# Performance work log

Measured on AMD Instinct MI355X. Metric: run time of the kernel, lower is better.

Reference implementation:

```python
import jax, jax.numpy as jnp
import numpy as np

VP = 0.4
EP = 0.21

def _c_matrix():
    # Faithfully replicate the original Ci (including its asymmetric rows 2) and invert.
    Ci = np.zeros((6, 6), dtype=np.float64)
    Ci[0, 0] = 1 / EP; Ci[0, 1] = -VP / EP; Ci[0, 2] = -VP / EP
    Ci[1, 0] = -VP / EP; Ci[1, 1] = 1 / EP; Ci[1, 2] = -VP / EP
    Ci[2, 0] = -VP;      Ci[2, 1] = -VP;      Ci[2, 2] = 1 / EP
    Ci[3, 3] = 2 * (1 + VP) / EP
    Ci[4, 4] = 2 * (1 + VP) / EP
    Ci[5, 5] = 2 * (1 + VP) / EP
    return np.linalg.inv(Ci).astype(np.float32)

C_MAT = jnp.asarray(_c_matrix())
N = 12288

def setup_inputs() -> dict:
    key = jax.random.key(0)
    k1, k2, k3 = jax.random.split(key, 3)
    xyz = jax.random.normal(k1, (N, 3), dtype=jnp.float32)
    new_xyz = jax.random.normal(k2, (N, 3), dtype=jnp.float32)
    # ~half the points are 'inside' (gt_sdf < 1e-8)
    gt_sdf = jax.random.uniform(k3, (N,), dtype=jnp.float32) - 0.5
    return {"new_xyz": new_xyz, "xyz": xyz, "gt_sdf": gt_sdf}

def reference(new_xyz, xyz, gt_sdf):
    motion = new_xyz - xyz                      # [N,3]
    inside = gt_sdf < 1e-8                      # [N] bool, selects inside points
    w = new_xyz                                 # warped coordinates (KNN space)
    n = w.shape[0]
    # Brute-force NN among inside points (KDTree k=2, second neighbor == nearest non-self).
    sq = jnp.sum(w * w, axis=1)                 # [N]
    d2 = sq[:, None] + sq[None, :] - 2.0 * (w @ w.T)   # [N,N] squared distances
    BIG = jnp.float32(1e30)
    bad_col = (~inside)[None, :] | jnp.eye(n, dtype=bool)
    d2 = jnp.where(bad_col, BIG, d2)
    nn_idx = jnp.argmin(d2, axis=1)             # nearest inside neighbor (excluding self)
    nn_d = jnp.sqrt(jnp.maximum(jnp.min(d2, axis=1), 0.0))
    # tree_list1 filter: drop rows whose nearest neighbor is a duplicate point
    valid = inside & (nn_d > 1e-8)              # [N]
    dm = motion[nn_idx] - motion                # motion_delta
    dc = w[nn_idx] - w + 1e-8                   # cords_delta (+1e-8 as in original)
    v = valid[:, None]
    dm = jnp.where(v, dm, 0.0)                  # neutralize masked rows (keep shapes static)
    dc = jnp.where(v, dc, 1.0)
    du, dv, dw = dm[:, 0], dm[:, 1], dm[:, 2]
    dx, dy, dz = dc[:, 0], dc[:, 1], dc[:, 2]
    et = jnp.stack([du / dx, dv / dy, dw / dz,
                    (du / dy + dv / dx) / 2,
                    (du / dz + dw / dx) / 2,
                    (dw / dy + dv / dz) / 2], axis=1)   # [N,6] strain tensor
    # diag(et @ C @ et.T) as an O(N) batched quadratic form
    q = jnp.einsum('ni,ij,nj->n', et, C_MAT, et)
    q = jnp.where(valid, q, 0.0)
    n_valid = jnp.sum(valid).astype(jnp.float32)
    return jnp.linalg.norm(q) / n_valid
```

## Files before the change

### kernel.cpp

```cpp
#include <hip/hip_runtime.h>
#include <math.h>
#include <string.h>

#define N 12288
#define QP 7168
#define TILE 128
#define NSPLIT 56
#define ACCS 2
#define QBLK 512
#define NQB 14
#define BT 1024
#define BB 12
#define NPART (QP / 256)

typedef unsigned long long ull;

struct CMat { float c[6][6]; };

__global__ __launch_bounds__(1024) void build_kernel(
    const float* __restrict__ new_xyz,
    const float* __restrict__ gt_sdf,
    float4* __restrict__ pts,
    int* __restrict__ cj,
    int* __restrict__ Mout,
    ull* __restrict__ best,
    unsigned int* __restrict__ ticket)
{
    const int tid = threadIdx.x;
    const int b = blockIdx.x;
    const int lane = tid & 63;
    const int wave = tid >> 6;

    int cpre = 0;
    #pragma unroll
    for (int r = 0; r < BB - 1; ++r) {
        const float sv = (r < b) ? gt_sdf[r * BT + tid] : 1.0f;
        cpre += (sv < 1e-8f) ? 1 : 0;
    }
    #pragma unroll
    for (int off = 32; off > 0; off >>= 1)
        cpre += __shfl_down(cpre, off, 64);

    const int idx = b * BT + tid;
    const float px = new_xyz[3 * idx + 0];
    const float py = new_xyz[3 * idx + 1];
    const float pz = new_xyz[3 * idx + 2];
    const bool ins = gt_sdf[idx] < 1e-8f;
    const ull m = __ballot(ins);
    const int rank = __popcll(m & ((1ull << lane) - 1ull));

    __shared__ int wpre[16];
    __shared__ int wcnt[16];
    __shared__ int woff[16];
    __shared__ int tot_s;
    if (lane == 0) { wpre[wave] = cpre; wcnt[wave] = __popcll(m); }
    __syncthreads();
    if (tid == 0) {
        int cb = 0;
        for (int w = 0; w < 16; ++w) cb += wpre[w];
        int run = cb;
        for (int w = 0; w < 16; ++w) { woff[w] = run; run += wcnt[w]; }
        tot_s = run;
    }
    __syncthreads();

    const int slot = woff[wave] + rank;
    if (ins && slot < QP) {
        pts[slot] = make_float4(-2.0f * px, -2.0f * py, -2.0f * pz,
                                px * px + py * py + pz * pz);
        cj[slot] = idx;
    }

    const int gid = b * BT + tid;
    if (gid < QP) best[gid] = ~0ull;
    if (gid == 0) *ticket = 0u;

    if (b == BB - 1) {
        const int M = tot_s;
        if (tid == 0) *Mout = M;
        for (int s = M + tid; s < QP; s += BT)
            pts[s] = make_float4(0.0f, 0.0f, 0.0f, 3e30f);
    }
}

template<bool CAREFUL>
__device__ __forceinline__ void nn_inner(
    const float4* __restrict__ tile,
    const float* wx, const float* wy, const float* wz,
    const int* kx,
    float* bd, int* bk)
{
    #pragma unroll 8
    for (int k = 0; k < TILE; ++k) {
        const float4 b = tile[k];
        #pragma unroll
        for (int a = 0; a < ACCS; ++a) {
            float t = fmaf(wz[a], b.z, b.w);
            t = fmaf(wy[a], b.y, t);
            t = fmaf(wx[a], b.x, t);
            bool ok = t < bd[a];
            if (CAREFUL) ok = ok && (k != kx[a]);
            if (ok) { bd[a] = t; bk[a] = k; }
        }
    }
}

__global__ __launch_bounds__(256, 4) void nn_kernel(
    const float4* __restrict__ pts,
    const int* __restrict__ Mptr,
    ull* __restrict__ best)
{
    const int tid = threadIdx.x;
    const int qbase = blockIdx.x * QBLK;
    const int s = blockIdx.y;
    const int jb = s * TILE;

    const int M = *Mptr;
    if (jb >= M || qbase >= M) return;

    float wx[ACCS], wy[ACCS], wz[ACCS];
    int kx[ACCS];
    #pragma unroll
    for (int a = 0; a < ACCS; ++a) {
        const int ci = qbase + tid + a * 256;
        const float4 q = pts[ci];
        wx[a] = -0.5f * q.x;
        wy[a] = -0.5f * q.y;
        wz[a] = -0.5f * q.z;
        kx[a] = ci - jb;
    }

    __shared__ float4 tile[TILE];
    if (tid < TILE) tile[tid] = pts[jb + tid];
    __syncthreads();

    float bd[ACCS];
    int bk[ACCS];
    #pragma unroll
    for (int a = 0; a < ACCS; ++a) { bd[a] = 3.0e38f; bk[a] = 0; }

    const bool dirty = (jb < qbase + QBLK) && (jb + TILE > qbase);
    if (dirty)
        nn_inner<true>(tile, wx, wy, wz, kx, bd, bk);
    else
        nn_inner<false>(tile, wx, wy, wz, kx, bd, bk);

    #pragma unroll
    for (int a = 0; a < ACCS; ++a) {
        const int ci = qbase + tid + a * 256;
        unsigned u = __float_as_uint(bd[a]);
        u = ((int)u < 0) ? ~u : (u | 0x80000000u);
        const ull v = ((ull)u << 32) | (ull)(unsigned)(jb + bk[a]);
        atomicMin(&best[ci], v);
    }
}

__global__ __launch_bounds__(256) void loss_kernel(
    const float* __restrict__ new_xyz,
    const float* __restrict__ xyz,
    const int* __restrict__ cj,
    const int* __restrict__ Mptr,
    const ull* __restrict__ best_arr,
    double* __restrict__ partial_sum,
    unsigned int* __restrict__ partial_cnt,
    unsigned int* __restrict__ ticket,
    float* __restrict__ out,
    CMat C)
{
    const int tid = threadIdx.x;
    const int ci = blockIdx.x * 256 + tid;

    const ull best = best_arr[ci];
    const int M = *Mptr;
    const bool real = (ci < M);

    const unsigned u = (unsigned)(best >> 32);
    const unsigned bits = (u & 0x80000000u) ? (u ^ 0x80000000u) : ~u;
    const float key = __uint_as_float(bits);
    const int cc = real ? (int)(unsigned)(best & 0xffffffffu) : 0;

    const int i  = real ? cj[ci] : 0;
    const int nn = cj[cc];

    const float wix = new_xyz[3 * i + 0];
    const float wiy = new_xyz[3 * i + 1];
    const float wiz = new_xyz[3 * i + 2];
    const float sqi = wix * wix + wiy * wiy + wiz * wiz;

    const float d2 = sqi + key;
    const float nnd = sqrtf(fmaxf(d2, 0.0f));
    const bool valid = real && (nnd > 1e-8f);

    float q = 0.0f;
    if (valid) {
        const float xix = xyz[3 * i + 0], xiy = xyz[3 * i + 1], xiz = xyz[3 * i + 2];
        const float wnx = new_xyz[3 * nn + 0], wny = new_xyz[3 * nn + 1], wnz = new_xyz[3 * nn + 2];
        const float xnx = xyz[3 * nn + 0],     xny = xyz[3 * nn + 1],     xnz = xyz[3 * nn + 2];

        const float du = (wnx - xnx) - (wix - xix);
        const float dv = (wny - xny) - (wiy - xiy);
        const float dw = (wnz - xnz) - (wiz - xiz);
        const float dx = wnx - wix + 1e-8f;
        const float dy = wny - wiy + 1e-8f;
        const float dz = wnz - wiz + 1e-8f;

        float et[6];
        et[0] = du / dx;
        et[1] = dv / dy;
        et[2] = dw / dz;
        et[3] = (du / dy + dv / dx) * 0.5f;
        et[4] = (du / dz + dw / dx) * 0.5f;
        et[5] = (dw / dy + dv / dz) * 0.5f;

        #pragma unroll
        for (int a = 0; a < 6; ++a) {
            float s2 = 0.0f;
            #pragma unroll
            for (int b2 = 0; b2 < 6; ++b2) s2 += C.c[a][b2] * et[b2];
            q += et[a] * s2;
        }
    }

    double q2 = (double)q * (double)q;
    #pragma unroll
    for (int off = 32; off > 0; off >>= 1)
        q2 += __shfl_down(q2, off, 64);
    const ull vm = __ballot(valid);
    const int lane = tid & 63;
    const int wid = tid >> 6;

    __shared__ double wsum[4];
    __shared__ unsigned wcnt2[4];
    __shared__ bool sdone;
    if (lane == 0) { wsum[wid] = q2; wcnt2[wid] = (unsigned)__popcll(vm); }
    __syncthreads();
    if (tid == 0) {
        partial_sum[blockIdx.x] = wsum[0] + wsum[1] + wsum[2] + wsum[3];
        partial_cnt[blockIdx.x] = wcnt2[0] + wcnt2[1] + wcnt2[2] + wcnt2[3];
        __threadfence();
        const unsigned t = atomicAdd(ticket, 1u);
        sdone = (t == NPART - 1);
    }
    __syncthreads();

    if (sdone && tid < 64) {
        __threadfence();
        double s = (tid < NPART) ? partial_sum[tid] : 0.0;
        double c = (tid < NPART) ? (double)partial_cnt[tid] : 0.0;
        #pragma unroll
        for (int off = 32; off > 0; off >>= 1) {
            s += __shfl_down(s, off, 64);
            c += __shfl_down(c, off, 64);
        }
        if (tid == 0) out[0] = (float)(sqrt(s) / c);
    }
}

static void build_cmat(CMat* M)
{
    const double VP = 0.4, EP = 0.21;
    double A[6][12];
    memset(A, 0, sizeof(A));
    double Ci[6][6];
    memset(Ci, 0, sizeof(Ci));
    Ci[0][0] = 1.0 / EP; Ci[0][1] = -VP / EP; Ci[0][2] = -VP / EP;
    Ci[1][0] = -VP / EP; Ci[1][1] = 1.0 / EP; Ci[1][2] = -VP / EP;
    Ci[2][0] = -VP;      Ci[2][1] = -VP;      Ci[2][2] = 1.0 / EP;
    Ci[3][3] = 2.0 * (1.0 + VP) / EP;
    Ci[4][4] = Ci[3][3];
    Ci[5][5] = Ci[3][3];

    for (int i = 0; i < 6; ++i) {
        for (int j = 0; j < 6; ++j) A[i][j] = Ci[i][j];
        A[i][6 + i] = 1.0;
    }
    for (int col = 0; col < 6; ++col) {
        int piv = col;
        for (int r = col + 1; r < 6; ++r)
            if (fabs(A[r][col]) > fabs(A[piv][col])) piv = r;
        if (piv != col)
            for (int c = 0; c < 12; ++c) { double t = A[col][c]; A[col][c] = A[piv][c]; A[piv][c] = t; }
        const double d = A[col][col];
        for (int c = 0; c < 12; ++c) A[col][c] /= d;
        for (int r = 0; r < 6; ++r) {
            if (r == col) continue;
            const double f = A[r][col];
            if (f == 0.0) continue;
            for (int c = 0; c < 12; ++c) A[r][c] -= f * A[col][c];
        }
    }
    for (int i = 0; i < 6; ++i)
        for (int j = 0; j < 6; ++j)
            M->c[i][j] = (float)A[i][6 + j];
}

extern "C" void kernel_launch(void* const* d_in, const int* in_sizes, int n_in,
                              void* d_out, int out_size, void* d_ws, size_t ws_size,
                              hipStream_t stream)
{
    const float* new_xyz = (const float*)d_in[0];
    const float* xyz     = (const float*)d_in[1];
    const float* gt_sdf  = (const float*)d_in[2];
    float* out = (float*)d_out;

    char* p = (char*)d_ws;
    float4* pts = (float4*)p;                    p += (size_t)QP * 16;
    int* cj = (int*)p;                           p += (size_t)QP * 4;
    int* Mptr = (int*)p;                         p += 16;
    ull* best = (ull*)p;                         p += (size_t)QP * 8;
    double* partial_sum = (double*)p;            p += NPART * sizeof(double);
    unsigned int* partial_cnt = (unsigned int*)p; p += NPART * sizeof(unsigned int);
    unsigned int* ticket = (unsigned int*)p;

    CMat C;
    build_cmat(&C);

    build_kernel<<<BB, BT, 0, stream>>>(new_xyz, gt_sdf, pts, cj, Mptr, best, ticket);
    nn_kernel<<<dim3(NQB, NSPLIT), 256, 0, stream>>>(pts, Mptr, best);
    loss_kernel<<<QP / 256, 256, 0, stream>>>(new_xyz, xyz, cj, Mptr, best,
                                              partial_sum, partial_cnt, ticket,
                                              out, C);
}
```

Baseline: 76.95 us.

## Fuse nearest-neighbour and loss kernels with a global-counter grid barrier

Merges the brute-force NN search kernel and the loss/reduction kernel into one launch. Every block increments a global ticket after its atomicMin updates, and the first NPART blocks spin-wait until all blocks have arrived before computing the loss. This removes one kernel launch and its inter-kernel gap. It relies on all blocks being co-resident and adds spin-wait traffic, with a guard that could break out early.

New measurement: 93.86 us. +22.0%, slower.

```diff
diff --git a/kernel.cpp b/kernel.cpp
--- a/kernel.cpp
+++ b/kernel.cpp
@@ -9,6 +9,7 @@
 #define ACCS 2
 #define QBLK 512
 #define NQB 14
+#define NBLK (NQB * NSPLIT)
 #define BT 1024
 #define BB 12
 #define NPART (QP / 256)
@@ -24,7 +25,8 @@
     int* __restrict__ cj,
     int* __restrict__ Mout,
     ull* __restrict__ best,
-    unsigned int* __restrict__ ticket)
+    unsigned int* __restrict__ ticket2,
+    unsigned int* __restrict__ ticket3)
 {
     const int tid = threadIdx.x;
     const int b = blockIdx.x;
@@ -73,7 +75,7 @@
 
     const int gid = b * BT + tid;
     if (gid < QP) best[gid] = ~0ull;
-    if (gid == 0) *ticket = 0u;
+    if (gid == 0) { *ticket2 = 0u; *ticket3 = 0u; }
 
     if (b == BB - 1) {
         const int M = tot_s;
@@ -105,79 +107,92 @@
     }
 }
 
-__global__ __launch_bounds__(256, 4) void nn_kernel(
-    const float4* __restrict__ pts,
-    const int* __restrict__ Mptr,
-    ull* __restrict__ best)
-{
-    const int tid = threadIdx.x;
-    const int qbase = blockIdx.x * QBLK;
-    const int s = blockIdx.y;
-    const int jb = s * TILE;
-
-    const int M = *Mptr;
-    if (jb >= M || qbase >= M) return;
-
-    float wx[ACCS], wy[ACCS], wz[ACCS];
-    int kx[ACCS];
-    #pragma unroll
-    for (int a = 0; a < ACCS; ++a) {
-        const int ci = qbase + tid + a * 256;
-        const float4 q = pts[ci];
-        wx[a] = -0.5f * q.x;
-        wy[a] = -0.5f * q.y;
-        wz[a] = -0.5f * q.z;
-        kx[a] = ci - jb;
-    }
-
-    __shared__ float4 tile[TILE];
-    if (tid < TILE) tile[tid] = pts[jb + tid];
-    __syncthreads();
-
-    float bd[ACCS];
-    int bk[ACCS];
-    #pragma unroll
-    for (int a = 0; a < ACCS; ++a) { bd[a] = 3.0e38f; bk[a] = 0; }
-
-    const bool dirty = (jb < qbase + QBLK) && (jb + TILE > qbase);
-    if (dirty)
-        nn_inner<true>(tile, wx, wy, wz, kx, bd, bk);
-    else
-        nn_inner<false>(tile, wx, wy, wz, kx, bd, bk);
-
-    #pragma unroll
-    for (int a = 0; a < ACCS; ++a) {
-        const int ci = qbase + tid + a * 256;
-        unsigned u = __float_as_uint(bd[a]);
-        u = ((int)u < 0) ? ~u : (u | 0x80000000u);
-        const ull v = ((ull)u << 32) | (ull)(unsigned)(jb + bk[a]);
-        atomicMin(&best[ci], v);
-    }
-}
-
-__global__ __launch_bounds__(256) void loss_kernel(
+__global__ __launch_bounds__(256, 4) void nn_loss_kernel(
     const float* __restrict__ new_xyz,
     const float* __restrict__ xyz,
+    const float4* __restrict__ pts,
     const int* __restrict__ cj,
     const int* __restrict__ Mptr,
-    const ull* __restrict__ best_arr,
+    ull* __restrict__ best,
+    unsigned int* __restrict__ ticket2,
+    unsigned int* __restrict__ ticket3,
     double* __restrict__ partial_sum,
     unsigned int* __restrict__ partial_cnt,
-    unsigned int* __restrict__ ticket,
     float* __restrict__ out,
     CMat C)
 {
     const int tid = threadIdx.x;
-    const int ci = blockIdx.x * 256 + tid;
-
-    const ull best = best_arr[ci];
+    const int f = blockIdx.x;
+    const int qb = f % NQB;
+    const int s = f / NQB;
+    const int qbase = qb * QBLK;
+    const int jb = s * TILE;
     const int M = *Mptr;
+
+    if (jb < M && qbase < M) {
+        float wx[ACCS], wy[ACCS], wz[ACCS];
+        int kx[ACCS];
+        #pragma unroll
+        for (int a = 0; a < ACCS; ++a) {
+            const int ci = qbase + tid + a * 256;
+            const float4 q = pts[ci];
+            wx[a] = -0.5f * q.x;
+            wy[a] = -0.5f * q.y;
+            wz[a] = -0.5f * q.z;
+            kx[a] = ci - jb;
+        }
+
+        __shared__ float4 tile[TILE];
+        if (tid < TILE) tile[tid] = pts[jb + tid];
+        __syncthreads();
+
+        float bd[ACCS];
+        int bk[ACCS];
+        #pragma unroll
+        for (int a = 0; a < ACCS; ++a) { bd[a] = 3.0e38f; bk[a] = 0; }
+
+        const bool dirty = (jb < qbase + QBLK) && (jb + TILE > qbase);
+        if (dirty)
+            nn_inner<true>(tile, wx, wy, wz, kx, bd, bk);
+        else
+            nn_inner<false>(tile, wx, wy, wz, kx, bd, bk);
+
+        #pragma unroll
+        for (int a = 0; a < ACCS; ++a) {
+            const int ci = qbase + tid + a * 256;
+            unsigned u = __float_as_uint(bd[a]);
+            u = ((int)u < 0) ? ~u : (u | 0x80000000u);
+            const ull v = ((ull)u << 32) | (ull)(unsigned)(jb + bk[a]);
+            atomicMin(&best[ci], v);
+        }
+    }
+
+    __syncthreads();
+    if (tid == 0) {
+        __threadfence();
+        __hip_atomic_fetch_add(ticket2, 1u, __ATOMIC_RELEASE,
+                               __HIP_MEMORY_SCOPE_AGENT);
+    }
+    if (f >= NPART) return;
+
+    if (tid == 0) {
+        long long guard = 0;
+        while (__hip_atomic_load(ticket2, __ATOMIC_ACQUIRE,
+                                 __HIP_MEMORY_SCOPE_AGENT) < (unsigned)NBLK) {
+            __builtin_amdgcn_s_sleep(8);
+            if (++guard > (1ll << 28)) break;
+        }
+    }
+    __syncthreads();
+
+    const int ci = f * 256 + tid;
+    const ull b64 = best[ci];
     const bool real = (ci < M);
 
-    const unsigned u = (unsigned)(best >> 32);
+    const unsigned u = (unsigned)(b64 >> 32);
     const unsigned bits = (u & 0x80000000u) ? (u ^ 0x80000000u) : ~u;
     const float key = __uint_as_float(bits);
-    const int cc = real ? (int)(unsigned)(best & 0xffffffffu) : 0;
+    const int cc = real ? (int)(unsigned)(b64 & 0xffffffffu) : 0;
 
     const int i  = real ? cj[ci] : 0;
     const int nn = cj[cc];
@@ -235,24 +250,24 @@
     if (lane == 0) { wsum[wid] = q2; wcnt2[wid] = (unsigned)__popcll(vm); }
     __syncthreads();
     if (tid == 0) {
-        partial_sum[blockIdx.x] = wsum[0] + wsum[1] + wsum[2] + wsum[3];
-        partial_cnt[blockIdx.x] = wcnt2[0] + wcnt2[1] + wcnt2[2] + wcnt2[3];
+        partial_sum[f] = wsum[0] + wsum[1] + wsum[2] + wsum[3];
+        partial_cnt[f] = wcnt2[0] + wcnt2[1] + wcnt2[2] + wcnt2[3];
         __threadfence();
-        const unsigned t = atomicAdd(ticket, 1u);
+        const unsigned t = atomicAdd(ticket3, 1u);
         sdone = (t == NPART - 1);
     }
     __syncthreads();
 
     if (sdone && tid < 64) {
         __threadfence();
-        double s = (tid < NPART) ? partial_sum[tid] : 0.0;
-        double c = (tid < NPART) ? (double)partial_cnt[tid] : 0.0;
+        double ss = (tid < NPART) ? partial_sum[tid] : 0.0;
+        double cc2 = (tid < NPART) ? (double)partial_cnt[tid] : 0.0;
         #pragma unroll
         for (int off = 32; off > 0; off >>= 1) {
-            s += __shfl_down(s, off, 64);
-            c += __shfl_down(c, off, 64);
-        }
-        if (tid == 0) out[0] = (float)(sqrt(s) / c);
+            ss += __shfl_down(ss, off, 64);
+            cc2 += __shfl_down(cc2, off, 64);
+        }
+        if (tid == 0) out[0] = (float)(sqrt(ss) / cc2);
     }
 }
 
@@ -310,14 +325,15 @@
     ull* best = (ull*)p;                         p += (size_t)QP * 8;
     double* partial_sum = (double*)p;            p += NPART * sizeof(double);
     unsigned int* partial_cnt = (unsigned int*)p; p += NPART * sizeof(unsigned int);
-    unsigned int* ticket = (unsigned int*)p;
+    unsigned int* ticket2 = (unsigned int*)p;    p += sizeof(unsigned int);
+    unsigned int* ticket3 = (unsigned int*)p;
 
     CMat C;
     build_cmat(&C);
 
-    build_kernel<<<BB, BT, 0, stream>>>(new_xyz, gt_sdf, pts, cj, Mptr, best, ticket);
-    nn_kernel<<<dim3(NQB, NSPLIT), 256, 0, stream>>>(pts, Mptr, best);
-    loss_kernel<<<QP / 256, 256, 0, stream>>>(new_xyz, xyz, cj, Mptr, best,
-                                              partial_sum, partial_cnt, ticket,
-                                              out, C);
-}
+    build_kernel<<<BB, BT, 0, stream>>>(new_xyz, gt_sdf, pts, cj, Mptr, best,
+                                        ticket2, ticket3);
+    nn_loss_kernel<<<NBLK, 256, 0, stream>>>(new_xyz, xyz, pts, cj, Mptr, best,
+                                             ticket2, ticket3,
+                                             partial_sum, partial_cnt, out, C);
+}
```

## Fuse NN search and loss into one kernel with per-block stripe reduction

Applied to the files above, without the earlier changes.

Merges the brute-force nearest-neighbour kernel and the loss kernel into a single launch. Each block now handles 32 queries, and 8 groups of 32 threads each scan a 896-point stripe, reading candidate points straight from global memory instead of a shared tile. Stripe results are reduced in shared memory, which removes the global atomicMin array, its initialisation and one kernel launch. The trade-off is fewer blocks (224) and one query per thread with no register reuse across queries, so the scan may be limited by memory latency or load throughput.

Measured after the change: 149.1 us. 93.7% more time.

```diff
diff --git a/kernel.cpp b/kernel.cpp
--- a/kernel.cpp
+++ b/kernel.cpp
@@ -4,14 +4,12 @@
 
 #define N 12288
 #define QP 7168
-#define TILE 128
-#define NSPLIT 56
-#define ACCS 2
-#define QBLK 512
-#define NQB 14
 #define BT 1024
 #define BB 12
-#define NPART (QP / 256)
+#define G2 224
+#define QG 32
+#define NST 8
+#define SL 896
 
 typedef unsigned long long ull;
 
@@ -23,7 +21,6 @@
     float4* __restrict__ pts,
     int* __restrict__ cj,
     int* __restrict__ Mout,
-    ull* __restrict__ best,
     unsigned int* __restrict__ ticket)
 {
     const int tid = threadIdx.x;
@@ -71,9 +68,7 @@
         cj[slot] = idx;
     }
 
-    const int gid = b * BT + tid;
-    if (gid < QP) best[gid] = ~0ull;
-    if (gid == 0) *ticket = 0u;
+    if (b == 0 && tid == 0) *ticket = 0u;
 
     if (b == BB - 1) {
         const int M = tot_s;
@@ -84,83 +79,28 @@
 }
 
 template<bool CAREFUL>
-__device__ __forceinline__ void nn_inner(
-    const float4* __restrict__ tile,
-    const float* wx, const float* wy, const float* wz,
-    const int* kx,
-    float* bd, int* bk)
+__device__ __forceinline__ void stripe_scan(
+    const float4* __restrict__ pts, int kb, int lim, int ci,
+    float wx, float wy, float wz, float* bd, int* bk)
 {
     #pragma unroll 8
-    for (int k = 0; k < TILE; ++k) {
-        const float4 b = tile[k];
-        #pragma unroll
-        for (int a = 0; a < ACCS; ++a) {
-            float t = fmaf(wz[a], b.z, b.w);
-            t = fmaf(wy[a], b.y, t);
-            t = fmaf(wx[a], b.x, t);
-            bool ok = t < bd[a];
-            if (CAREFUL) ok = ok && (k != kx[a]);
-            if (ok) { bd[a] = t; bk[a] = k; }
-        }
-    }
-}
-
-__global__ __launch_bounds__(256, 4) void nn_kernel(
-    const float4* __restrict__ pts,
-    const int* __restrict__ Mptr,
-    ull* __restrict__ best)
-{
-    const int tid = threadIdx.x;
-    const int qbase = blockIdx.x * QBLK;
-    const int s = blockIdx.y;
-    const int jb = s * TILE;
-
-    const int M = *Mptr;
-    if (jb >= M || qbase >= M) return;
-
-    float wx[ACCS], wy[ACCS], wz[ACCS];
-    int kx[ACCS];
-    #pragma unroll
-    for (int a = 0; a < ACCS; ++a) {
-        const int ci = qbase + tid + a * 256;
-        const float4 q = pts[ci];
-        wx[a] = -0.5f * q.x;
-        wy[a] = -0.5f * q.y;
-        wz[a] = -0.5f * q.z;
-        kx[a] = ci - jb;
-    }
-
-    __shared__ float4 tile[TILE];
-    if (tid < TILE) tile[tid] = pts[jb + tid];
-    __syncthreads();
-
-    float bd[ACCS];
-    int bk[ACCS];
-    #pragma unroll
-    for (int a = 0; a < ACCS; ++a) { bd[a] = 3.0e38f; bk[a] = 0; }
-
-    const bool dirty = (jb < qbase + QBLK) && (jb + TILE > qbase);
-    if (dirty)
-        nn_inner<true>(tile, wx, wy, wz, kx, bd, bk);
-    else
-        nn_inner<false>(tile, wx, wy, wz, kx, bd, bk);
-
-    #pragma unroll
-    for (int a = 0; a < ACCS; ++a) {
-        const int ci = qbase + tid + a * 256;
-        unsigned u = __float_as_uint(bd[a]);
-        u = ((int)u < 0) ? ~u : (u | 0x80000000u);
-        const ull v = ((ull)u << 32) | (ull)(unsigned)(jb + bk[a]);
-        atomicMin(&best[ci], v);
-    }
-}
-
-__global__ __launch_bounds__(256) void loss_kernel(
+    for (int k = 0; k < lim; ++k) {
+        const float4 b = pts[kb + k];
+        float t = fmaf(wz, b.z, b.w);
+        t = fmaf(wy, b.y, t);
+        t = fmaf(wx, b.x, t);
+        bool ok = t < *bd;
+        if (CAREFUL) ok = ok && (kb + k != ci);
+        if (ok) { *bd = t; *bk = k; }
+    }
+}
+
+__global__ __launch_bounds__(256, 4) void nnloss_kernel(
     const float* __restrict__ new_xyz,
     const float* __restrict__ xyz,
+    const float4* __restrict__ pts,
     const int* __restrict__ cj,
     const int* __restrict__ Mptr,
-    const ull* __restrict__ best_arr,
     double* __restrict__ partial_sum,
     unsigned int* __restrict__ partial_cnt,
     unsigned int* __restrict__ ticket,
@@ -168,85 +108,132 @@
     CMat C)
 {
     const int tid = threadIdx.x;
-    const int ci = blockIdx.x * 256 + tid;
-
-    const ull best = best_arr[ci];
+    const int g = blockIdx.x;
+    const int lane = tid & 63;
+    const int qi = tid & 31;
+    const int st = tid >> 5;
+    const int qbase = g * QG;
     const int M = *Mptr;
-    const bool real = (ci < M);
-
-    const unsigned u = (unsigned)(best >> 32);
-    const unsigned bits = (u & 0x80000000u) ? (u ^ 0x80000000u) : ~u;
-    const float key = __uint_as_float(bits);
-    const int cc = real ? (int)(unsigned)(best & 0xffffffffu) : 0;
-
-    const int i  = real ? cj[ci] : 0;
-    const int nn = cj[cc];
-
-    const float wix = new_xyz[3 * i + 0];
-    const float wiy = new_xyz[3 * i + 1];
-    const float wiz = new_xyz[3 * i + 2];
-    const float sqi = wix * wix + wiy * wiy + wiz * wiz;
-
-    const float d2 = sqi + key;
-    const float nnd = sqrtf(fmaxf(d2, 0.0f));
-    const bool valid = real && (nnd > 1e-8f);
-
-    float q = 0.0f;
-    if (valid) {
-        const float xix = xyz[3 * i + 0], xiy = xyz[3 * i + 1], xiz = xyz[3 * i + 2];
-        const float wnx = new_xyz[3 * nn + 0], wny = new_xyz[3 * nn + 1], wnz = new_xyz[3 * nn + 2];
-        const float xnx = xyz[3 * nn + 0],     xny = xyz[3 * nn + 1],     xnz = xyz[3 * nn + 2];
-
-        const float du = (wnx - xnx) - (wix - xix);
-        const float dv = (wny - xny) - (wiy - xiy);
-        const float dw = (wnz - xnz) - (wiz - xiz);
-        const float dx = wnx - wix + 1e-8f;
-        const float dy = wny - wiy + 1e-8f;
-        const float dz = wnz - wiz + 1e-8f;
-
-        float et[6];
-        et[0] = du / dx;
-        et[1] = dv / dy;
-        et[2] = dw / dz;
-        et[3] = (du / dy + dv / dx) * 0.5f;
-        et[4] = (du / dz + dw / dx) * 0.5f;
-        et[5] = (dw / dy + dv / dz) * 0.5f;
+    const bool active = (qbase < M);
+
+    __shared__ ull sb[NST][QG];
+    __shared__ bool sdone;
+
+    if (active) {
+        const int ci = qbase + qi;
+        const float4 q = pts[ci];
+        const float wx = -0.5f * q.x;
+        const float wy = -0.5f * q.y;
+        const float wz = -0.5f * q.z;
+
+        float bd = 3.0e38f;
+        int bk = 0;
+        const int kb = st * SL;
+        int lim = M - kb;
+        lim = (lim > SL) ? SL : lim;
+
+        if (st == qbase / SL)
+            stripe_scan<true>(pts, kb, lim, ci, wx, wy, wz, &bd, &bk);
+        else
+            stripe_scan<false>(pts, kb, lim, ci, wx, wy, wz, &bd, &bk);
+
+        unsigned u = __float_as_uint(bd);
+        u = ((int)u < 0) ? ~u : (u | 0x80000000u);
+        sb[st][qi] = ((ull)u << 32) | (ull)(unsigned)(kb + bk);
+    }
+    __syncthreads();
+
+    double red = 0.0;
+    unsigned cnt = 0;
+    if (tid < 64) {
+        double q2 = 0.0;
+        bool valid = false;
+        if (active && lane < 32) {
+            const int ci = qbase + lane;
+            ull best = sb[0][lane];
+            #pragma unroll
+            for (int s2 = 1; s2 < NST; ++s2) {
+                const ull p = sb[s2][lane];
+                best = (p < best) ? p : best;
+            }
+
+            const bool real = (ci < M);
+            const unsigned u = (unsigned)(best >> 32);
+            const unsigned bits = (u & 0x80000000u) ? (u ^ 0x80000000u) : ~u;
+            const float key = __uint_as_float(bits);
+            const int cc = real ? (int)(unsigned)(best & 0xffffffffu) : 0;
+
+            const int i  = real ? cj[ci] : 0;
+            const int nn = cj[cc];
+
+            const float wix = new_xyz[3 * i + 0];
+            const float wiy = new_xyz[3 * i + 1];
+            const float wiz = new_xyz[3 * i + 2];
+            const float sqi = wix * wix + wiy * wiy + wiz * wiz;
+
+            const float d2 = sqi + key;
+            const float nnd = sqrtf(fmaxf(d2, 0.0f));
+            valid = real && (nnd > 1e-8f);
+
+            float qv = 0.0f;
+            if (valid) {
+                const float xix = xyz[3 * i + 0], xiy = xyz[3 * i + 1], xiz = xyz[3 * i + 2];
+                const float wnx = new_xyz[3 * nn + 0], wny = new_xyz[3 * nn + 1], wnz = new_xyz[3 * nn + 2];
+                const float xnx = xyz[3 * nn + 0],     xny = xyz[3 * nn + 1],     xnz = xyz[3 * nn + 2];
+
+                const float du = (wnx - xnx) - (wix - xix);
+                const float dv = (wny - xny) - (wiy - xiy);
+                const float dw = (wnz - xnz) - (wiz - xiz);
+                const float dx = wnx - wix + 1e-8f;
+                const float dy = wny - wiy + 1e-8f;
+                const float dz = wnz - wiz + 1e-8f;
+
+                float et[6];
+                et[0] = du / dx;
+                et[1] = dv / dy;
+                et[2] = dw / dz;
+                et[3] = (du / dy + dv / dx) * 0.5f;
+                et[4] = (du / dz + dw / dx) * 0.5f;
+                et[5] = (dw / dy + dv / dz) * 0.5f;
+
+                #pragma unroll
+                for (int a = 0; a < 6; ++a) {
+                    float s2 = 0.0f;
+                    #pragma unroll
+                    for (int b2 = 0; b2 < 6; ++b2) s2 += C.c[a][b2] * et[b2];
+                    qv += et[a] * s2;
+                }
+            }
+            q2 = (double)qv * (double)qv;
+        }
 
         #pragma unroll
-        for (int a = 0; a < 6; ++a) {
-            float s2 = 0.0f;
-            #pragma unroll
-            for (int b2 = 0; b2 < 6; ++b2) s2 += C.c[a][b2] * et[b2];
-            q += et[a] * s2;
-        }
-    }
-
-    double q2 = (double)q * (double)q;
-    #pragma unroll
-    for (int off = 32; off > 0; off >>= 1)
-        q2 += __shfl_down(q2, off, 64);
-    const ull vm = __ballot(valid);
-    const int lane = tid & 63;
-    const int wid = tid >> 6;
-
-    __shared__ double wsum[4];
-    __shared__ unsigned wcnt2[4];
-    __shared__ bool sdone;
-    if (lane == 0) { wsum[wid] = q2; wcnt2[wid] = (unsigned)__popcll(vm); }
-    __syncthreads();
+        for (int off = 32; off > 0; off >>= 1)
+            q2 += __shfl_down(q2, off, 64);
+        red = q2;
+        cnt = (unsigned)__popcll(__ballot(valid));
+    }
+
     if (tid == 0) {
-        partial_sum[blockIdx.x] = wsum[0] + wsum[1] + wsum[2] + wsum[3];
-        partial_cnt[blockIdx.x] = wcnt2[0] + wcnt2[1] + wcnt2[2] + wcnt2[3];
+        partial_sum[g] = red;
+        partial_cnt[g] = cnt;
         __threadfence();
         const unsigned t = atomicAdd(ticket, 1u);
-        sdone = (t == NPART - 1);
+        sdone = (t == G2 - 1);
     }
     __syncthreads();
 
     if (sdone && tid < 64) {
         __threadfence();
-        double s = (tid < NPART) ? partial_sum[tid] : 0.0;
-        double c = (tid < NPART) ? (double)partial_cnt[tid] : 0.0;
+        double s = 0.0, c = 0.0;
+        #pragma unroll
+        for (int j = 0; j < 4; ++j) {
+            const int idx = tid * 4 + j;
+            if (idx < G2) {
+                s += partial_sum[idx];
+                c += (double)partial_cnt[idx];
+            }
+        }
         #pragma unroll
         for (int off = 32; off > 0; off >>= 1) {
             s += __shfl_down(s, off, 64);
@@ -307,17 +294,15 @@
     float4* pts = (float4*)p;                    p += (size_t)QP * 16;
     int* cj = (int*)p;                           p += (size_t)QP * 4;
     int* Mptr = (int*)p;                         p += 16;
-    ull* best = (ull*)p;                         p += (size_t)QP * 8;
-    double* partial_sum = (double*)p;            p += NPART * sizeof(double);
-    unsigned int* partial_cnt = (unsigned int*)p; p += NPART * sizeof(unsigned int);
+    double* partial_sum = (double*)p;            p += G2 * sizeof(double);
+    unsigned int* partial_cnt = (unsigned int*)p; p += G2 * sizeof(unsigned int);
     unsigned int* ticket = (unsigned int*)p;
 
     CMat C;
     build_cmat(&C);
 
-    build_kernel<<<BB, BT, 0, stream>>>(new_xyz, gt_sdf, pts, cj, Mptr, best, ticket);
-    nn_kernel<<<dim3(NQB, NSPLIT), 256, 0, stream>>>(pts, Mptr, best);
-    loss_kernel<<<QP / 256, 256, 0, stream>>>(new_xyz, xyz, cj, Mptr, best,
-                                              partial_sum, partial_cnt, ticket,
-                                              out, C);
-}
+    build_kernel<<<BB, BT, 0, stream>>>(new_xyz, gt_sdf, pts, cj, Mptr, ticket);
+    nnloss_kernel<<<G2, 256, 0, stream>>>(new_xyz, xyz, pts, cj, Mptr,
+                                          partial_sum, partial_cnt, ticket,
+                                          out, C);
+}
```
